# Kernel optimization log

Hardware: AMD Instinct MI355X
Metric: run time of the kernel (lower is better)

Reference implementation:

```python
import jax, jax.numpy as jnp
import numpy as np

OBS_DIM = 256
ACTION_DIM = 4
NUM_OBJECTS = 16
HIDDEN = 512
BATCH = 4096
LN_EPS = 1e-5


def _uniform(key, shape, stdv):
    return jax.random.uniform(key, shape, jnp.float32, -stdv, stdv)


def setup_inputs() -> dict:
    key = jax.random.key(0)
    ks = jax.random.split(key, 8)
    node_in = OBS_DIM + ACTION_DIM
    s1 = 1.0 / np.sqrt(HIDDEN)
    s3 = 1.0 / np.sqrt(OBS_DIM)
    return {
        "states": jax.random.normal(ks[0], (BATCH, NUM_OBJECTS, OBS_DIM), jnp.float32),
        "action": jax.random.randint(ks[1], (BATCH,), 0, ACTION_DIM * NUM_OBJECTS, jnp.int64 if jax.config.jax_enable_x64 else jnp.int32),
        "W1": _uniform(ks[2], (node_in, HIDDEN), s1),
        "b1": _uniform(ks[3], (HIDDEN,), s1),
        "W2": _uniform(ks[4], (HIDDEN, HIDDEN), s1),
        "b2": _uniform(ks[5], (HIDDEN,), s1),
        "W3": _uniform(ks[6], (HIDDEN, OBS_DIM), s3),
        "b3": _uniform(ks[7], (OBS_DIM,), s3),
        "ln_g": jnp.ones((HIDDEN,), jnp.float32),
        "ln_b": jnp.zeros((HIDDEN,), jnp.float32),
    }


def _gc(x, W, b):
    # x: [B, O, d_in]. adj = block_diag(ones(O,O)/O) == per-graph mean pooling,
    # broadcast back to every node in the graph.
    s = jnp.einsum("bod,dh->boh", x, W)
    m = jnp.mean(s, axis=1, keepdims=True)  # [B, 1, h]
    return jnp.broadcast_to(m, s.shape) + b


def _layernorm(x, g, b):
    mu = jnp.mean(x, axis=-1, keepdims=True)
    var = jnp.mean(jnp.square(x - mu), axis=-1, keepdims=True)
    return (x - mu) * jax.lax.rsqrt(var + LN_EPS) * g + b


def reference(states, action, W1, b1, W2, b2, W3, b3, ln_g, ln_b):
    B, O, D = states.shape
    # one_hot(action, A*O).view(-1, A) == per-node one-hot slices
    a = jax.nn.one_hot(action, ACTION_DIM * O, dtype=states.dtype)
    a = a.reshape(B, O, ACTION_DIM)
    x = jnp.concatenate([states, a], axis=-1)  # [B, O, D+A]
    h = jax.nn.relu(_gc(x, W1, b1))
    h = jax.nn.relu(_layernorm(_gc(h, W2, b2), ln_g, ln_b))
    out = _gc(h, W3, b3)  # [B, O, obs_dim]
    return out
```

## Files before the change

### kernel.cpp

```cpp
#include <hip/hip_runtime.h>
#include <hip/hip_bf16.h>

#define BSZ   4096
#define NOBJ  16
#define DOBS  256
#define ADIM  4
#define HID   512
#define KP1   288

typedef unsigned short u16;
typedef __bf16 bf16x8 __attribute__((ext_vector_type(8)));
typedef float  f32x4  __attribute__((ext_vector_type(4)));
typedef unsigned short u16x8 __attribute__((ext_vector_type(8)));

static __device__ __forceinline__ u16 f2bf(float f) {
    __hip_bfloat16 h = __float2bfloat16(f);
    return __builtin_bit_cast(u16, h);
}

__global__ void prep_weights(const float* __restrict__ W1, const float* __restrict__ W2,
                             const float* __restrict__ W3,
                             u16* __restrict__ W1T, u16* __restrict__ W2T, u16* __restrict__ W3T) {
    int idx = blockIdx.x * 256 + threadIdx.x;
    const int n1 = HID * KP1;
    const int n2 = HID * HID;
    const int n3 = DOBS * HID;
    if (idx < n1) {
        int h = idx / KP1, k = idx % KP1;
        float v = (k < DOBS + ADIM) ? W1[k * HID + h] : 0.0f;
        W1T[idx] = f2bf(v);
    } else if (idx < n1 + n2) {
        int t = idx - n1;
        int h = t / HID, k = t % HID;
        W2T[t] = f2bf(W2[k * HID + h]);
    } else if (idx < n1 + n2 + n3) {
        int t = idx - n1 - n2;
        int n = t / HID, k = t % HID;
        W3T[t] = f2bf(W3[k * DOBS + n]);
    }
}

__global__ void reduce_states(const float* __restrict__ states, const int* __restrict__ action,
                              u16* __restrict__ xbar) {
    int b = blockIdx.x;
    int d = threadIdx.x;
    const float* sp = states + (size_t)b * (NOBJ * DOBS) + d;
    float s = 0.f;
#pragma unroll
    for (int o = 0; o < NOBJ; ++o) s += sp[o * DOBS];
    xbar[(size_t)b * KP1 + d] = f2bf(s * (1.0f / NOBJ));
    if (d < KP1 - DOBS) {
        int a = action[b] & 3;
        float v = (d == a) ? (1.0f / NOBJ) : 0.0f;
        xbar[(size_t)b * KP1 + DOBS + d] = f2bf(v);
    }
}

template <int EPI>
__global__ __launch_bounds__(256) void gemm_mfma(const u16* __restrict__ A, int lda,
                                                 const u16* __restrict__ BT, int ldb,
                                                 const float* __restrict__ bias,
                                                 void* __restrict__ outp, int ldo, int ksteps) {
    int w  = threadIdx.x >> 6;
    int l  = threadIdx.x & 63;
    int lr = l & 15;
    int lg = l >> 4;
    int m0 = blockIdx.x * 64 + w * 16;
    int n0 = blockIdx.y * 64;

    const u16* ap = A  + (size_t)(m0 + lr) * lda + lg * 8;
    const u16* bp = BT + (size_t)(n0 + lr) * ldb + lg * 8;

    f32x4 acc[4] = {};
    for (int ks = 0; ks < ksteps; ++ks) {
        bf16x8 a = __builtin_bit_cast(bf16x8, *(const u16x8*)ap);
#pragma unroll
        for (int nb = 0; nb < 4; ++nb) {
            bf16x8 bv = __builtin_bit_cast(bf16x8, *(const u16x8*)(bp + (size_t)nb * 16 * ldb));
            acc[nb] = __builtin_amdgcn_mfma_f32_16x16x32_bf16(a, bv, acc[nb], 0, 0, 0);
        }
        ap += 32;
        bp += 32;
    }

#pragma unroll
    for (int nb = 0; nb < 4; ++nb) {
        int gn = n0 + nb * 16 + lr;
        float bvl = bias[gn];
#pragma unroll
        for (int r = 0; r < 4; ++r) {
            int gm = m0 + lg * 4 + r;
            float v = acc[nb][r] + bvl;
            if (EPI == 0) {
                v = fmaxf(v, 0.f);
                ((u16*)outp)[(size_t)gm * ldo + gn] = f2bf(v);
            } else if (EPI == 1) {
                ((float*)outp)[(size_t)gm * ldo + gn] = v;
            } else {
                float* op = (float*)outp + (size_t)gm * (NOBJ * DOBS) + gn;
#pragma unroll
                for (int o = 0; o < NOBJ; ++o) op[o * DOBS] = v;
            }
        }
    }
}

__global__ __launch_bounds__(256) void ln_relu(const float* __restrict__ t2,
                                               const float* __restrict__ g,
                                               const float* __restrict__ bb,
                                               u16* __restrict__ h2) {
    int b = blockIdx.x;
    int t = threadIdx.x;
    const float* row = t2 + (size_t)b * HID;
    float x0 = row[t], x1 = row[t + 256];
    float s1 = x0 + x1;
    float s2 = x0 * x0 + x1 * x1;
#pragma unroll
    for (int m = 32; m; m >>= 1) {
        s1 += __shfl_xor(s1, m, 64);
        s2 += __shfl_xor(s2, m, 64);
    }
    __shared__ float ls1[4], ls2[4];
    int w = t >> 6;
    if ((t & 63) == 0) { ls1[w] = s1; ls2[w] = s2; }
    __syncthreads();
    s1 = ls1[0] + ls1[1] + ls1[2] + ls1[3];
    s2 = ls2[0] + ls2[1] + ls2[2] + ls2[3];
    float mu  = s1 * (1.0f / HID);
    float var = s2 * (1.0f / HID) - mu * mu;
    float rs  = rsqrtf(var + 1e-5f);
    float y0 = fmaxf((x0 - mu) * rs * g[t]       + bb[t],       0.f);
    float y1 = fmaxf((x1 - mu) * rs * g[t + 256] + bb[t + 256], 0.f);
    h2[(size_t)b * HID + t]       = f2bf(y0);
    h2[(size_t)b * HID + t + 256] = f2bf(y1);
}

extern "C" void kernel_launch(void* const* d_in, const int* in_sizes, int n_in,
                              void* d_out, int out_size, void* d_ws, size_t ws_size,
                              hipStream_t stream) {
    const float* states = (const float*)d_in[0];
    const int*   action = (const int*)d_in[1];
    const float* W1 = (const float*)d_in[2];
    const float* b1 = (const float*)d_in[3];
    const float* W2 = (const float*)d_in[4];
    const float* b2 = (const float*)d_in[5];
    const float* W3 = (const float*)d_in[6];
    const float* b3 = (const float*)d_in[7];
    const float* lng = (const float*)d_in[8];
    const float* lnb = (const float*)d_in[9];
    float* out = (float*)d_out;

    char* ws = (char*)d_ws;
    size_t off = 0;
    auto alloc = [&](size_t bytes) -> void* {
        void* p = ws + off;
        off = (off + bytes + 255) & ~(size_t)255;
        return p;
    };
    u16*   W1T  = (u16*)alloc((size_t)HID * KP1 * 2);
    u16*   W2T  = (u16*)alloc((size_t)HID * HID * 2);
    u16*   W3T  = (u16*)alloc((size_t)DOBS * HID * 2);
    u16*   xbar = (u16*)alloc((size_t)BSZ * KP1 * 2);
    u16*   h1   = (u16*)alloc((size_t)BSZ * HID * 2);
    float* t2   = (float*)alloc((size_t)BSZ * HID * 4);
    u16*   h2   = (u16*)alloc((size_t)BSZ * HID * 2);

    prep_weights<<<2112, 256, 0, stream>>>(W1, W2, W3, W1T, W2T, W3T);
    reduce_states<<<BSZ, 256, 0, stream>>>(states, action, xbar);
    gemm_mfma<0><<<dim3(BSZ / 64, HID / 64), 256, 0, stream>>>(xbar, KP1, W1T, KP1, b1, h1, HID, KP1 / 32);
    gemm_mfma<1><<<dim3(BSZ / 64, HID / 64), 256, 0, stream>>>(h1, HID, W2T, HID, b2, t2, HID, HID / 32);
    ln_relu<<<BSZ, 256, 0, stream>>>(t2, lng, lnb, h2);
    gemm_mfma<2><<<dim3(BSZ / 64, DOBS / 64), 256, 0, stream>>>(h2, HID, W3T, HID, b3, out, 0, HID / 32);
}
```

Before: 184.4 us.

## Fuse state reduction, three GEMMs, and LayerNorm into one per-batch-tile kernel

Replaces the reduce, three GEMM, and LayerNorm kernels with one kernel. Each block handles 16 batch rows and keeps the pooled input, hidden activations and LayerNorm statistics in shared memory. This removes the global round trips for xbar, h1, t2 and h2 and several launches, and the output broadcast now uses float4 stores staged in LDS. The cost is that each block streams the full weight matrices from global/L2, with only 256 blocks and heavy LDS use, so weight bandwidth and occupancy may limit it.

```diff
diff --git a/kernel.cpp b/kernel.cpp
--- a/kernel.cpp
+++ b/kernel.cpp
@@ -8,6 +8,11 @@
 #define HID   512
 #define KP1   288
 
+#define MB    16
+#define XP1   296
+#define HP    520
+#define TP    260
+
 typedef unsigned short u16;
 typedef __bf16 bf16x8 __attribute__((ext_vector_type(8)));
 typedef float  f32x4  __attribute__((ext_vector_type(4)));
@@ -16,6 +21,9 @@
 static __device__ __forceinline__ u16 f2bf(float f) {
     __hip_bfloat16 h = __float2bfloat16(f);
     return __builtin_bit_cast(u16, h);
+}
+static __device__ __forceinline__ bf16x8 ldg8(const u16* p) {
+    return __builtin_bit_cast(bf16x8, *(const u16x8*)p);
 }
 
 __global__ void prep_weights(const float* __restrict__ W1, const float* __restrict__ W2,
@@ -40,99 +48,164 @@
     }
 }
 
-__global__ void reduce_states(const float* __restrict__ states, const int* __restrict__ action,
-                              u16* __restrict__ xbar) {
-    int b = blockIdx.x;
-    int d = threadIdx.x;
-    const float* sp = states + (size_t)b * (NOBJ * DOBS) + d;
-    float s = 0.f;
-#pragma unroll
-    for (int o = 0; o < NOBJ; ++o) s += sp[o * DOBS];
-    xbar[(size_t)b * KP1 + d] = f2bf(s * (1.0f / NOBJ));
-    if (d < KP1 - DOBS) {
-        int a = action[b] & 3;
-        float v = (d == a) ? (1.0f / NOBJ) : 0.0f;
-        xbar[(size_t)b * KP1 + DOBS + d] = f2bf(v);
-    }
-}
-
-template <int EPI>
-__global__ __launch_bounds__(256) void gemm_mfma(const u16* __restrict__ A, int lda,
-                                                 const u16* __restrict__ BT, int ldb,
-                                                 const float* __restrict__ bias,
-                                                 void* __restrict__ outp, int ldo, int ksteps) {
-    int w  = threadIdx.x >> 6;
-    int l  = threadIdx.x & 63;
-    int lr = l & 15;
-    int lg = l >> 4;
-    int m0 = blockIdx.x * 64 + w * 16;
-    int n0 = blockIdx.y * 64;
-
-    const u16* ap = A  + (size_t)(m0 + lr) * lda + lg * 8;
-    const u16* bp = BT + (size_t)(n0 + lr) * ldb + lg * 8;
-
-    f32x4 acc[4] = {};
-    for (int ks = 0; ks < ksteps; ++ks) {
-        bf16x8 a = __builtin_bit_cast(bf16x8, *(const u16x8*)ap);
-#pragma unroll
+__global__ __launch_bounds__(256) void fused_mlp(
+    const float* __restrict__ states, const int* __restrict__ action,
+    const u16* __restrict__ W1T, const float* __restrict__ b1,
+    const u16* __restrict__ W2T, const float* __restrict__ b2,
+    const u16* __restrict__ W3T, const float* __restrict__ b3,
+    const float* __restrict__ lng, const float* __restrict__ lnb,
+    float* __restrict__ out)
+{
+    __shared__ u16   xbar[MB][XP1];
+    __shared__ u16   h1[MB][HP];
+    __shared__ u16   h2[MB][HP];
+    __shared__ float t3[MB][TP];
+    __shared__ float red[2][4][MB];
+
+    const int t  = threadIdx.x;
+    const int w  = t >> 6;
+    const int l  = t & 63;
+    const int lr = l & 15;
+    const int lg = l >> 4;
+    const int b0 = blockIdx.x * MB;
+
+    {
+        const int d = t;
+        #pragma unroll 4
+        for (int r = 0; r < MB; ++r) {
+            const float* sp = states + ((size_t)(b0 + r) * NOBJ) * DOBS + d;
+            float s = 0.f;
+            #pragma unroll
+            for (int o = 0; o < NOBJ; ++o) s += sp[o * DOBS];
+            xbar[r][d] = f2bf(s * (1.0f / NOBJ));
+        }
+        if (t < MB) {
+            int a = action[b0 + t] & 3;
+            #pragma unroll
+            for (int k = 0; k < KP1 - DOBS; ++k)
+                xbar[t][DOBS + k] = f2bf(k == a ? (1.0f / NOBJ) : 0.0f);
+        }
+    }
+    __syncthreads();
+
+    {
+        f32x4 acc[8] = {};
+        #pragma unroll 3
+        for (int ks = 0; ks < KP1 / 32; ++ks) {
+            bf16x8 a = ldg8(&xbar[lr][ks * 32 + lg * 8]);
+            #pragma unroll
+            for (int nb = 0; nb < 8; ++nb) {
+                int n = w * 128 + nb * 16 + lr;
+                bf16x8 bv = ldg8(W1T + (size_t)n * KP1 + ks * 32 + lg * 8);
+                acc[nb] = __builtin_amdgcn_mfma_f32_16x16x32_bf16(a, bv, acc[nb], 0, 0, 0);
+            }
+        }
+        #pragma unroll
+        for (int nb = 0; nb < 8; ++nb) {
+            int n = w * 128 + nb * 16 + lr;
+            float bias = b1[n];
+            #pragma unroll
+            for (int r = 0; r < 4; ++r)
+                h1[lg * 4 + r][n] = f2bf(fmaxf(acc[nb][r] + bias, 0.f));
+        }
+    }
+    __syncthreads();
+
+    {
+        f32x4 acc[8] = {};
+        #pragma unroll 4
+        for (int ks = 0; ks < HID / 32; ++ks) {
+            bf16x8 a = ldg8(&h1[lr][ks * 32 + lg * 8]);
+            #pragma unroll
+            for (int nb = 0; nb < 8; ++nb) {
+                int n = w * 128 + nb * 16 + lr;
+                bf16x8 bv = ldg8(W2T + (size_t)n * HID + ks * 32 + lg * 8);
+                acc[nb] = __builtin_amdgcn_mfma_f32_16x16x32_bf16(a, bv, acc[nb], 0, 0, 0);
+            }
+        }
+        float s1[4] = {0.f, 0.f, 0.f, 0.f}, s2[4] = {0.f, 0.f, 0.f, 0.f};
+        #pragma unroll
+        for (int nb = 0; nb < 8; ++nb) {
+            float bias = b2[w * 128 + nb * 16 + lr];
+            #pragma unroll
+            for (int r = 0; r < 4; ++r) {
+                float v = acc[nb][r] + bias;
+                acc[nb][r] = v;
+                s1[r] += v;
+                s2[r] += v * v;
+            }
+        }
+        #pragma unroll
+        for (int r = 0; r < 4; ++r) {
+            #pragma unroll
+            for (int m = 8; m; m >>= 1) {
+                s1[r] += __shfl_xor(s1[r], m, 64);
+                s2[r] += __shfl_xor(s2[r], m, 64);
+            }
+            if (lr == 0) {
+                red[0][w][lg * 4 + r] = s1[r];
+                red[1][w][lg * 4 + r] = s2[r];
+            }
+        }
+        __syncthreads();
+        float muv[4], rsv[4];
+        #pragma unroll
+        for (int r = 0; r < 4; ++r) {
+            int m = lg * 4 + r;
+            float S1 = red[0][0][m] + red[0][1][m] + red[0][2][m] + red[0][3][m];
+            float S2 = red[1][0][m] + red[1][1][m] + red[1][2][m] + red[1][3][m];
+            float mu = S1 * (1.0f / HID);
+            float var = S2 * (1.0f / HID) - mu * mu;
+            muv[r] = mu;
+            rsv[r] = rsqrtf(var + 1e-5f);
+        }
+        #pragma unroll
+        for (int nb = 0; nb < 8; ++nb) {
+            int n = w * 128 + nb * 16 + lr;
+            float g = lng[n], bb = lnb[n];
+            #pragma unroll
+            for (int r = 0; r < 4; ++r) {
+                float y = (acc[nb][r] - muv[r]) * rsv[r] * g + bb;
+                h2[lg * 4 + r][n] = f2bf(fmaxf(y, 0.f));
+            }
+        }
+    }
+    __syncthreads();
+
+    {
+        f32x4 acc[4] = {};
+        #pragma unroll 4
+        for (int ks = 0; ks < HID / 32; ++ks) {
+            bf16x8 a = ldg8(&h2[lr][ks * 32 + lg * 8]);
+            #pragma unroll
+            for (int nb = 0; nb < 4; ++nb) {
+                int n = w * 64 + nb * 16 + lr;
+                bf16x8 bv = ldg8(W3T + (size_t)n * HID + ks * 32 + lg * 8);
+                acc[nb] = __builtin_amdgcn_mfma_f32_16x16x32_bf16(a, bv, acc[nb], 0, 0, 0);
+            }
+        }
+        #pragma unroll
         for (int nb = 0; nb < 4; ++nb) {
-            bf16x8 bv = __builtin_bit_cast(bf16x8, *(const u16x8*)(bp + (size_t)nb * 16 * ldb));
-            acc[nb] = __builtin_amdgcn_mfma_f32_16x16x32_bf16(a, bv, acc[nb], 0, 0, 0);
-        }
-        ap += 32;
-        bp += 32;
-    }
-
-#pragma unroll
-    for (int nb = 0; nb < 4; ++nb) {
-        int gn = n0 + nb * 16 + lr;
-        float bvl = bias[gn];
-#pragma unroll
-        for (int r = 0; r < 4; ++r) {
-            int gm = m0 + lg * 4 + r;
-            float v = acc[nb][r] + bvl;
-            if (EPI == 0) {
-                v = fmaxf(v, 0.f);
-                ((u16*)outp)[(size_t)gm * ldo + gn] = f2bf(v);
-            } else if (EPI == 1) {
-                ((float*)outp)[(size_t)gm * ldo + gn] = v;
-            } else {
-                float* op = (float*)outp + (size_t)gm * (NOBJ * DOBS) + gn;
-#pragma unroll
-                for (int o = 0; o < NOBJ; ++o) op[o * DOBS] = v;
-            }
-        }
-    }
-}
-
-__global__ __launch_bounds__(256) void ln_relu(const float* __restrict__ t2,
-                                               const float* __restrict__ g,
-                                               const float* __restrict__ bb,
-                                               u16* __restrict__ h2) {
-    int b = blockIdx.x;
-    int t = threadIdx.x;
-    const float* row = t2 + (size_t)b * HID;
-    float x0 = row[t], x1 = row[t + 256];
-    float s1 = x0 + x1;
-    float s2 = x0 * x0 + x1 * x1;
-#pragma unroll
-    for (int m = 32; m; m >>= 1) {
-        s1 += __shfl_xor(s1, m, 64);
-        s2 += __shfl_xor(s2, m, 64);
-    }
-    __shared__ float ls1[4], ls2[4];
-    int w = t >> 6;
-    if ((t & 63) == 0) { ls1[w] = s1; ls2[w] = s2; }
-    __syncthreads();
-    s1 = ls1[0] + ls1[1] + ls1[2] + ls1[3];
-    s2 = ls2[0] + ls2[1] + ls2[2] + ls2[3];
-    float mu  = s1 * (1.0f / HID);
-    float var = s2 * (1.0f / HID) - mu * mu;
-    float rs  = rsqrtf(var + 1e-5f);
-    float y0 = fmaxf((x0 - mu) * rs * g[t]       + bb[t],       0.f);
-    float y1 = fmaxf((x1 - mu) * rs * g[t + 256] + bb[t + 256], 0.f);
-    h2[(size_t)b * HID + t]       = f2bf(y0);
-    h2[(size_t)b * HID + t + 256] = f2bf(y1);
+            int n = w * 64 + nb * 16 + lr;
+            float bias = b3[n];
+            #pragma unroll
+            for (int r = 0; r < 4; ++r)
+                t3[lg * 4 + r][n] = acc[nb][r] + bias;
+        }
+    }
+    __syncthreads();
+
+    {
+        #pragma unroll 4
+        for (int i = 0; i < 64; ++i) {
+            int flat = i * 256 + t;
+            int d4 = flat & 63;
+            int o  = (flat >> 6) & 15;
+            int r  = flat >> 10;
+            float4 v = *(const float4*)&t3[r][d4 * 4];
+            *(float4*)(out + ((size_t)(b0 + r) * NOBJ + o) * DOBS + d4 * 4) = v;
+        }
+    }
 }
 
 extern "C" void kernel_launch(void* const* d_in, const int* in_sizes, int n_in,
@@ -157,18 +230,12 @@
         off = (off + bytes + 255) & ~(size_t)255;
         return p;
     };
-    u16*   W1T  = (u16*)alloc((size_t)HID * KP1 * 2);
-    u16*   W2T  = (u16*)alloc((size_t)HID * HID * 2);
-    u16*   W3T  = (u16*)alloc((size_t)DOBS * HID * 2);
-    u16*   xbar = (u16*)alloc((size_t)BSZ * KP1 * 2);
-    u16*   h1   = (u16*)alloc((size_t)BSZ * HID * 2);
-    float* t2   = (float*)alloc((size_t)BSZ * HID * 4);
-    u16*   h2   = (u16*)alloc((size_t)BSZ * HID * 2);
+    u16* W1T = (u16*)alloc((size_t)HID * KP1 * 2);
+    u16* W2T = (u16*)alloc((size_t)HID * HID * 2);
+    u16* W3T = (u16*)alloc((size_t)DOBS * HID * 2);
 
     prep_weights<<<2112, 256, 0, stream>>>(W1, W2, W3, W1T, W2T, W3T);
-    reduce_states<<<BSZ, 256, 0, stream>>>(states, action, xbar);
-    gemm_mfma<0><<<dim3(BSZ / 64, HID / 64), 256, 0, stream>>>(xbar, KP1, W1T, KP1, b1, h1, HID, KP1 / 32);
-    gemm_mfma<1><<<dim3(BSZ / 64, HID / 64), 256, 0, stream>>>(h1, HID, W2T, HID, b2, t2, HID, HID / 32);
-    ln_relu<<<BSZ, 256, 0, stream>>>(t2, lng, lnb, h2);
-    gemm_mfma<2><<<dim3(BSZ / 64, DOBS / 64), 256, 0, stream>>>(h2, HID, W3T, HID, b3, out, 0, HID / 32);
-}
+    fused_mlp<<<BSZ / MB, 256, 0, stream>>>(states, action,
+                                            W1T, b1, W2T, b2, W3T, b3,
+                                            lng, lnb, out);
+}
```

New measurement: 161.3 us. 12.5% less time.
